# Optimization experiments

Measured on AMD Instinct MI355X. Metric: run time of the kernel, lower is better.

Reference implementation:

```python
import jax, jax.numpy as jnp
import numpy as np

# Module config (from init_kwargs): causal=False, window_size=(256,256), window_type=0,
# softmax_scale=None -> 1/sqrt(D), dropout=0 (eval mode).
WINDOW_LEFT, WINDOW_RIGHT = 256, 256


def _window_mask(Sq, Sk, causal, use_window_mask):
    """Boolean [Sq, Sk] visibility mask, FA2 semantics (right-aligned offset)."""
    qi = jnp.arange(Sq)[:, None]
    kj = jnp.arange(Sk)[None, :]
    offset = Sk - Sq
    if causal:
        return kj <= qi + offset  # window (-1, 0)
    if use_window_mask:
        m = jnp.ones((Sq, Sk), dtype=bool)
        if WINDOW_LEFT >= 0:
            m = m & (kj >= qi + offset - WINDOW_LEFT)
        if WINDOW_RIGHT >= 0:
            m = m & (kj <= qi + offset + WINDOW_RIGHT)
        return m
    return None  # full attention


def setup_inputs() -> dict:
    key = jax.random.key(0)
    kq, kkv = jax.random.split(key)
    B, Sq, Sk, H, D = 2, 2048, 2048, 16, 64
    q = jax.random.normal(kq, (B, Sq, H, D), dtype=jnp.float32)
    kv = jax.random.normal(kkv, (B, Sk, 2, H, D), dtype=jnp.float32)
    return {"q": q, "kv": kv, "causal": 0, "use_window_mask": 1, "return_attn_probs": 0}


def reference(q, kv, causal, use_window_mask, return_attn_probs):
    # q: (B, Sq, H, D); kv: (B, Sk, 2, H, D)
    B, Sq, H, D = q.shape
    Sk = kv.shape[1]
    k = kv[:, :, 0]  # (B, Sk, H, D)
    v = kv[:, :, 1]
    scale = 1.0 / (D ** 0.5)
    scores = jnp.einsum('bqhd,bkhd->bhqk', q, k) * scale  # (B, H, Sq, Sk)
    mask = _window_mask(Sq, Sk, bool(causal), bool(use_window_mask))
    if mask is not None:
        scores = jnp.where(mask[None, None], scores, jnp.finfo(scores.dtype).min)
    probs = jax.nn.softmax(scores, axis=-1)
    out = jnp.einsum('bhqk,bkhd->bqhd', probs, v)  # (B, Sq, H, D)
    return out
```

## Files before the change

### kernel.cpp

```cpp
#include <hip/hip_runtime.h>
#include <hip/hip_bf16.h>

#define B_    2
#define SQ_   2048
#define SK_   2048
#define NH_   16
#define DH_   64
#define WIN_  256
#define NEG_  -30000.0f

typedef __bf16 bf16_t;
typedef bf16_t bf16x8 __attribute__((ext_vector_type(8)));
typedef bf16_t bf16x4 __attribute__((ext_vector_type(4)));
typedef float  f32x4  __attribute__((ext_vector_type(4)));
typedef short  s16x4  __attribute__((ext_vector_type(4)));

#define KSTRIDE 72
#define VSTRIDE 72

__global__ __launch_bounds__(256, 4)
void fa_fwd(const float* __restrict__ qg, const float* __restrict__ kvg,
            float* __restrict__ outg) {
  const int tid  = threadIdx.x;
  const int wid  = tid >> 6;
  const int lane = tid & 63;
  const int quad = lane >> 4;
  const int li   = lane & 15;

  const int bid = blockIdx.x;
  const int qb  = bid >> 5;
  const int bh  = bid & 31;
  const int b   = bh >> 4;
  const int h   = bh & 15;

  const int q0b = qb * 64;
  const int q0  = q0b + wid * 16;

  __shared__ __align__(16) bf16_t sK [2][64 * KSTRIDE];
  __shared__ __align__(16) bf16_t sVT[2][64 * VSTRIDE];

  const float qscale = 0.125f * 1.44269504088896340736f;
  const float* qrow = qg + ((size_t)((b * SQ_ + q0 + li) * NH_ + h)) * DH_;
  bf16x8 qfrag[2];
#pragma unroll
  for (int c = 0; c < 2; ++c) {
    f32x4 a0 = *(const f32x4*)(qrow + c * 32 + quad * 8);
    f32x4 a1 = *(const f32x4*)(qrow + c * 32 + quad * 8 + 4);
#pragma unroll
    for (int i = 0; i < 4; ++i) {
      qfrag[c][i]     = (bf16_t)(a0[i] * qscale);
      qfrag[c][i + 4] = (bf16_t)(a1[i] * qscale);
    }
  }

  f32x4 oacc[4];
#pragma unroll
  for (int t = 0; t < 4; ++t) { f32x4 z = {0.f, 0.f, 0.f, 0.f}; oacc[t] = z; }
  float m = NEG_, l = 0.f;

  int klo = q0b - WIN_; if (klo < 0) klo = 0;
  int khi = q0b + 63 + WIN_ + 1; if (khi > SK_) khi = SK_;
  const int nt = (khi - klo + 63) >> 6;

  const float* kbase = kvg + (size_t)b * SK_ * 2 * NH_ * DH_ + (size_t)h * DH_;
  const float* vbase = kbase + NH_ * DH_;
  const size_t krow_stride = 2 * NH_ * DH_;

  const int skey = tid >> 2;
  const int sd0  = (tid & 3) * 16;

  f32x4 ka[4], va[4];

  auto issue_loads = [&](int kt) {
    const float* kr = kbase + (size_t)(kt + skey) * krow_stride + sd0;
    const float* vr = vbase + (size_t)(kt + skey) * krow_stride + sd0;
#pragma unroll
    for (int i = 0; i < 4; ++i) {
      ka[i] = *(const f32x4*)(kr + 4 * i);
      va[i] = *(const f32x4*)(vr + 4 * i);
    }
  };

  auto stage = [&](int bb) {
#pragma unroll
    for (int hh = 0; hh < 2; ++hh) {
      bf16x8 wk;
#pragma unroll
      for (int i = 0; i < 4; ++i) {
        wk[i] = (bf16_t)ka[2 * hh][i]; wk[i + 4] = (bf16_t)ka[2 * hh + 1][i];
      }
      *(bf16x8*)(&sK[bb][skey * KSTRIDE + sd0 + 8 * hh]) = wk;
      const int dbase = sd0 + 8 * hh;
      const int vcol  = skey ^ (((dbase >> 3) & 7) << 3);
#pragma unroll
      for (int i = 0; i < 4; ++i) {
        sVT[bb][(dbase + i)     * VSTRIDE + vcol] = (bf16_t)va[2 * hh][i];
        sVT[bb][(dbase + 4 + i) * VSTRIDE + vcol] = (bf16_t)va[2 * hh + 1][i];
      }
    }
  };

  issue_loads(klo);
  stage(0);
  if (nt > 1) issue_loads(klo + 64);
  __syncthreads();

  int buf = 0;
  for (int t = 0; t < nt; ++t) {
    const int kk = klo + t * 64;
    if (t + 1 < nt) stage(buf ^ 1);
    if (t + 2 < nt) issue_loads(klo + (t + 2) * 64);

    if (kk + 63 >= q0 - WIN_ && kk <= q0 + 15 + WIN_) {
      f32x4 sc[4];
      __builtin_amdgcn_s_setprio(1);
#pragma unroll
      for (int s = 0; s < 4; ++s) {
        bf16x8 kf0 = *(const bf16x8*)(&sK[buf][(s * 16 + li) * KSTRIDE + quad * 8]);
        bf16x8 kf1 = *(const bf16x8*)(&sK[buf][(s * 16 + li) * KSTRIDE + 32 + quad * 8]);
        f32x4 acc = {0.f, 0.f, 0.f, 0.f};
        acc = __builtin_amdgcn_mfma_f32_16x16x32_bf16(kf0, qfrag[0], acc, 0, 0, 0);
        acc = __builtin_amdgcn_mfma_f32_16x16x32_bf16(kf1, qfrag[1], acc, 0, 0, 0);
        sc[s] = acc;
      }
      __builtin_amdgcn_s_setprio(0);
      if (kk < q0 - 241 || kk > q0 + 193) {
        const int qa = q0 + li;
#pragma unroll
        for (int s = 0; s < 4; ++s)
#pragma unroll
          for (int r = 0; r < 4; ++r) {
            int key = kk + s * 16 + quad * 4 + r;
            unsigned dd = (unsigned)(key - qa + WIN_);
            if (dd > 2u * WIN_) sc[s][r] = NEG_;
          }
      }
      float tl = NEG_;
#pragma unroll
      for (int s = 0; s < 4; ++s)
        tl = fmaxf(tl, fmaxf(fmaxf(sc[s][0], sc[s][1]), fmaxf(sc[s][2], sc[s][3])));

      const bool defer = (__all(tl <= m + 8.0f) != 0);
      float mnew = m;
      if (!defer) {
        float tr = fmaxf(tl, __shfl_xor(tl, 16));
        tr = fmaxf(tr, __shfl_xor(tr, 32));
        mnew = fmaxf(m, tr);
      }

      float psum = 0.f;
      bf16x4 pa[4];
#pragma unroll
      for (int s = 0; s < 4; ++s) {
        float p0 = exp2f(sc[s][0] - mnew);
        float p1 = exp2f(sc[s][1] - mnew);
        float p2 = exp2f(sc[s][2] - mnew);
        float p3 = exp2f(sc[s][3] - mnew);
        psum += (p0 + p1) + (p2 + p3);
        pa[s][0] = (bf16_t)p0; pa[s][1] = (bf16_t)p1;
        pa[s][2] = (bf16_t)p2; pa[s][3] = (bf16_t)p3;
      }

      if (!defer) {
        const float alpha = exp2f(m - mnew);
        float al[4];
#pragma unroll
        for (int r = 0; r < 4; ++r) al[r] = __shfl(alpha, quad * 4 + r);
#pragma unroll
        for (int t2 = 0; t2 < 4; ++t2) {
          oacc[t2][0] *= al[0]; oacc[t2][1] *= al[1];
          oacc[t2][2] *= al[2]; oacc[t2][3] *= al[3];
        }
        l = l * alpha + psum;
        m = mnew;
      } else {
        l += psum;
      }

      __builtin_amdgcn_s_setprio(1);
#pragma unroll
      for (int s = 0; s < 4; ++s) {
        const s16x4 pas = __builtin_bit_cast(s16x4, pa[s]);
#pragma unroll
        for (int t2 = 0; t2 < 4; ++t2) {
          const int d  = 16 * t2 + li;
          const int c8 = ((2 * t2 + (li >> 3)) & 7) << 3;
          s16x4 vb = *(const s16x4*)(&sVT[buf][d * VSTRIDE + ((s * 16 + quad * 4) ^ c8)]);
          oacc[t2] = __builtin_amdgcn_mfma_f32_16x16x16bf16_1k(pas, vb, oacc[t2], 0, 0, 0);
        }
      }
      __builtin_amdgcn_s_setprio(0);
    }

    __syncthreads();
    buf ^= 1;
  }

  l += __shfl_xor(l, 16);
  l += __shfl_xor(l, 32);
  float rl[4];
#pragma unroll
  for (int r = 0; r < 4; ++r) {
    float lv = __shfl(l, quad * 4 + r);
    rl[r] = 1.0f / lv;
  }
  float* orow = outg + ((size_t)((b * SQ_ + q0) * NH_ + h)) * DH_;
#pragma unroll
  for (int t = 0; t < 4; ++t)
#pragma unroll
    for (int r = 0; r < 4; ++r)
      orow[(size_t)(quad * 4 + r) * (NH_ * DH_) + 16 * t + li] = oacc[t][r] * rl[r];
}

extern "C" void kernel_launch(void* const* d_in, const int* in_sizes, int n_in,
                              void* d_out, int out_size, void* d_ws, size_t ws_size,
                              hipStream_t stream) {
  (void)in_sizes; (void)n_in; (void)out_size; (void)d_ws; (void)ws_size;
  const float* q  = (const float*)d_in[0];
  const float* kv = (const float*)d_in[1];
  float* out = (float*)d_out;
  dim3 grid(B_ * NH_ * (SQ_ / 64));
  fa_fwd<<<grid, 256, 0, stream>>>(q, kv, out);
}
```

Baseline: 117.7 us.

## Switch to 32x32x16 MFMA tiles with 128-query blocks and LDS-staged P

Each wave now handles 32 query rows using 32x32x16 bf16 MFMAs for both QK^T and PV, and each block covers 128 queries instead of 64. The P matrix is written to a per-wave LDS buffer and reloaded in operand layout for the PV product. This halves the grid and improves K/V reuse per staged tile while using larger matrix instructions. The cost is extra LDS traffic for P, a lgkmcnt wait, more registers (launch bounds lowered to 2 blocks), and fewer blocks to fill the GPU.

```diff
diff --git a/kernel.cpp b/kernel.cpp
--- a/kernel.cpp
+++ b/kernel.cpp
@@ -13,19 +13,27 @@
 typedef bf16_t bf16x8 __attribute__((ext_vector_type(8)));
 typedef bf16_t bf16x4 __attribute__((ext_vector_type(4)));
 typedef float  f32x4  __attribute__((ext_vector_type(4)));
-typedef short  s16x4  __attribute__((ext_vector_type(4)));
+typedef float  f32x16 __attribute__((ext_vector_type(16)));
 
 #define KSTRIDE 72
 #define VSTRIDE 72
-
-__global__ __launch_bounds__(256, 4)
+#define PSTRIDE 72
+
+static __device__ __forceinline__ f32x16 zero16() {
+  f32x16 z;
+#pragma unroll
+  for (int i = 0; i < 16; ++i) z[i] = 0.f;
+  return z;
+}
+
+__global__ __launch_bounds__(256, 2)
 void fa_fwd(const float* __restrict__ qg, const float* __restrict__ kvg,
             float* __restrict__ outg) {
   const int tid  = threadIdx.x;
   const int wid  = tid >> 6;
   const int lane = tid & 63;
-  const int quad = lane >> 4;
-  const int li   = lane & 15;
+  const int c31  = lane & 31;
+  const int hi   = lane >> 5;
 
   const int bid = blockIdx.x;
   const int qb  = bid >> 5;
@@ -33,33 +41,35 @@
   const int b   = bh >> 4;
   const int h   = bh & 15;
 
-  const int q0b = qb * 64;
-  const int q0  = q0b + wid * 16;
+  const int q0b = qb * 128;
+  const int q0  = q0b + wid * 32;
 
   __shared__ __align__(16) bf16_t sK [2][64 * KSTRIDE];
   __shared__ __align__(16) bf16_t sVT[2][64 * VSTRIDE];
+  __shared__ __align__(16) bf16_t sP [4][32 * PSTRIDE];
+  bf16_t* plw = sP[wid];
 
   const float qscale = 0.125f * 1.44269504088896340736f;
-  const float* qrow = qg + ((size_t)((b * SQ_ + q0 + li) * NH_ + h)) * DH_;
-  bf16x8 qfrag[2];
-#pragma unroll
-  for (int c = 0; c < 2; ++c) {
-    f32x4 a0 = *(const f32x4*)(qrow + c * 32 + quad * 8);
-    f32x4 a1 = *(const f32x4*)(qrow + c * 32 + quad * 8 + 4);
+  const float* qrow = qg + ((size_t)((b * SQ_ + q0 + c31) * NH_ + h)) * DH_;
+  bf16x8 qfrag[4];
+#pragma unroll
+  for (int ds = 0; ds < 4; ++ds) {
+    const int d0 = ds * 16 + hi * 8;
+    f32x4 a0 = *(const f32x4*)(qrow + d0);
+    f32x4 a1 = *(const f32x4*)(qrow + d0 + 4);
 #pragma unroll
     for (int i = 0; i < 4; ++i) {
-      qfrag[c][i]     = (bf16_t)(a0[i] * qscale);
-      qfrag[c][i + 4] = (bf16_t)(a1[i] * qscale);
+      qfrag[ds][i]     = (bf16_t)(a0[i] * qscale);
+      qfrag[ds][i + 4] = (bf16_t)(a1[i] * qscale);
     }
   }
 
-  f32x4 oacc[4];
-#pragma unroll
-  for (int t = 0; t < 4; ++t) { f32x4 z = {0.f, 0.f, 0.f, 0.f}; oacc[t] = z; }
-  float m = NEG_, l = 0.f;
+  f32x16 oacc[2];
+  oacc[0] = zero16(); oacc[1] = zero16();
+  float m = NEG_, el = 0.f;
 
   int klo = q0b - WIN_; if (klo < 0) klo = 0;
-  int khi = q0b + 63 + WIN_ + 1; if (khi > SK_) khi = SK_;
+  int khi = q0b + 127 + WIN_ + 1; if (khi > SK_) khi = SK_;
   const int nt = (khi - klo + 63) >> 6;
 
   const float* kbase = kvg + (size_t)b * SK_ * 2 * NH_ * DH_ + (size_t)h * DH_;
@@ -111,82 +121,96 @@
     if (t + 1 < nt) stage(buf ^ 1);
     if (t + 2 < nt) issue_loads(klo + (t + 2) * 64);
 
-    if (kk + 63 >= q0 - WIN_ && kk <= q0 + 15 + WIN_) {
-      f32x4 sc[4];
+    if (kk + 63 >= q0 - WIN_ && kk <= q0 + 31 + WIN_) {
+      f32x16 sc[2];
       __builtin_amdgcn_s_setprio(1);
 #pragma unroll
-      for (int s = 0; s < 4; ++s) {
-        bf16x8 kf0 = *(const bf16x8*)(&sK[buf][(s * 16 + li) * KSTRIDE + quad * 8]);
-        bf16x8 kf1 = *(const bf16x8*)(&sK[buf][(s * 16 + li) * KSTRIDE + 32 + quad * 8]);
-        f32x4 acc = {0.f, 0.f, 0.f, 0.f};
-        acc = __builtin_amdgcn_mfma_f32_16x16x32_bf16(kf0, qfrag[0], acc, 0, 0, 0);
-        acc = __builtin_amdgcn_mfma_f32_16x16x32_bf16(kf1, qfrag[1], acc, 0, 0, 0);
-        sc[s] = acc;
+      for (int kh = 0; kh < 2; ++kh) {
+        f32x16 acc = zero16();
+#pragma unroll
+        for (int ds = 0; ds < 4; ++ds) {
+          bf16x8 kf = *(const bf16x8*)(
+              &sK[buf][(kh * 32 + c31) * KSTRIDE + ds * 16 + hi * 8]);
+          acc = __builtin_amdgcn_mfma_f32_32x32x16_bf16(kf, qfrag[ds], acc, 0, 0, 0);
+        }
+        sc[kh] = acc;
       }
       __builtin_amdgcn_s_setprio(0);
-      if (kk < q0 - 241 || kk > q0 + 193) {
-        const int qa = q0 + li;
-#pragma unroll
-        for (int s = 0; s < 4; ++s)
-#pragma unroll
-          for (int r = 0; r < 4; ++r) {
-            int key = kk + s * 16 + quad * 4 + r;
+
+      if (kk < q0 - 225 || kk > q0 + 193) {
+        const int qa = q0 + c31;
+#pragma unroll
+        for (int kh = 0; kh < 2; ++kh)
+#pragma unroll
+          for (int r = 0; r < 16; ++r) {
+            int key = kk + kh * 32 + (r & 3) + 8 * (r >> 2) + 4 * hi;
             unsigned dd = (unsigned)(key - qa + WIN_);
-            if (dd > 2u * WIN_) sc[s][r] = NEG_;
+            if (dd > 2u * WIN_) sc[kh][r] = NEG_;
           }
       }
+
       float tl = NEG_;
 #pragma unroll
-      for (int s = 0; s < 4; ++s)
-        tl = fmaxf(tl, fmaxf(fmaxf(sc[s][0], sc[s][1]), fmaxf(sc[s][2], sc[s][3])));
+      for (int kh = 0; kh < 2; ++kh)
+#pragma unroll
+        for (int r = 0; r < 16; r += 4)
+          tl = fmaxf(tl, fmaxf(fmaxf(sc[kh][r], sc[kh][r + 1]),
+                               fmaxf(sc[kh][r + 2], sc[kh][r + 3])));
 
       const bool defer = (__all(tl <= m + 8.0f) != 0);
       float mnew = m;
       if (!defer) {
-        float tr = fmaxf(tl, __shfl_xor(tl, 16));
-        tr = fmaxf(tr, __shfl_xor(tr, 32));
+        float tr = fmaxf(tl, __shfl_xor(tl, 32));
         mnew = fmaxf(m, tr);
       }
 
       float psum = 0.f;
-      bf16x4 pa[4];
-#pragma unroll
-      for (int s = 0; s < 4; ++s) {
-        float p0 = exp2f(sc[s][0] - mnew);
-        float p1 = exp2f(sc[s][1] - mnew);
-        float p2 = exp2f(sc[s][2] - mnew);
-        float p3 = exp2f(sc[s][3] - mnew);
-        psum += (p0 + p1) + (p2 + p3);
-        pa[s][0] = (bf16_t)p0; pa[s][1] = (bf16_t)p1;
-        pa[s][2] = (bf16_t)p2; pa[s][3] = (bf16_t)p3;
-      }
+#pragma unroll
+      for (int kh = 0; kh < 2; ++kh)
+#pragma unroll
+        for (int g = 0; g < 4; ++g) {
+          float p0 = exp2f(sc[kh][4 * g + 0] - mnew);
+          float p1 = exp2f(sc[kh][4 * g + 1] - mnew);
+          float p2 = exp2f(sc[kh][4 * g + 2] - mnew);
+          float p3 = exp2f(sc[kh][4 * g + 3] - mnew);
+          psum += (p0 + p1) + (p2 + p3);
+          bf16x4 pk;
+          pk[0] = (bf16_t)p0; pk[1] = (bf16_t)p1;
+          pk[2] = (bf16_t)p2; pk[3] = (bf16_t)p3;
+          *(bf16x4*)(&plw[c31 * PSTRIDE + kh * 32 + g * 8 + hi * 4]) = pk;
+        }
 
       if (!defer) {
-        const float alpha = exp2f(m - mnew);
-        float al[4];
-#pragma unroll
-        for (int r = 0; r < 4; ++r) al[r] = __shfl(alpha, quad * 4 + r);
-#pragma unroll
-        for (int t2 = 0; t2 < 4; ++t2) {
-          oacc[t2][0] *= al[0]; oacc[t2][1] *= al[1];
-          oacc[t2][2] *= al[2]; oacc[t2][3] *= al[3];
-        }
-        l = l * alpha + psum;
+        const float alq = exp2f(m - mnew);
+#pragma unroll
+        for (int r = 0; r < 16; ++r) {
+          const int row = (r & 3) + 8 * (r >> 2) + 4 * hi;
+          const float al = __shfl(alq, row);
+          oacc[0][r] *= al; oacc[1][r] *= al;
+        }
+        el = el * alq + psum;
         m = mnew;
       } else {
-        l += psum;
-      }
+        el += psum;
+      }
+
+      asm volatile("s_waitcnt lgkmcnt(0)" ::: "memory");
+
+      bf16x8 pf[4];
+#pragma unroll
+      for (int ks = 0; ks < 4; ++ks)
+        pf[ks] = *(const bf16x8*)(&plw[c31 * PSTRIDE + ks * 16 + hi * 8]);
 
       __builtin_amdgcn_s_setprio(1);
 #pragma unroll
-      for (int s = 0; s < 4; ++s) {
-        const s16x4 pas = __builtin_bit_cast(s16x4, pa[s]);
-#pragma unroll
-        for (int t2 = 0; t2 < 4; ++t2) {
-          const int d  = 16 * t2 + li;
-          const int c8 = ((2 * t2 + (li >> 3)) & 7) << 3;
-          s16x4 vb = *(const s16x4*)(&sVT[buf][d * VSTRIDE + ((s * 16 + quad * 4) ^ c8)]);
-          oacc[t2] = __builtin_amdgcn_mfma_f32_16x16x16bf16_1k(pas, vb, oacc[t2], 0, 0, 0);
+      for (int dt = 0; dt < 2; ++dt) {
+        const int d  = dt * 32 + c31;
+        const int c8 = ((d >> 3) & 7) << 3;
+#pragma unroll
+        for (int ks = 0; ks < 4; ++ks) {
+          bf16x8 vf = *(const bf16x8*)(
+              &sVT[buf][d * VSTRIDE + ((ks * 16 + hi * 8) ^ c8)]);
+          oacc[dt] = __builtin_amdgcn_mfma_f32_32x32x16_bf16(pf[ks], vf, oacc[dt], 0, 0, 0);
         }
       }
       __builtin_amdgcn_s_setprio(0);
@@ -196,20 +220,17 @@
     buf ^= 1;
   }
 
-  l += __shfl_xor(l, 16);
-  l += __shfl_xor(l, 32);
-  float rl[4];
-#pragma unroll
-  for (int r = 0; r < 4; ++r) {
-    float lv = __shfl(l, quad * 4 + r);
-    rl[r] = 1.0f / lv;
+  el += __shfl_xor(el, 32);
+  const float rlq = 1.0f / el;
+#pragma unroll
+  for (int r = 0; r < 16; ++r) {
+    const int row = (r & 3) + 8 * (r >> 2) + 4 * hi;
+    const float rl = __shfl(rlq, row);
+    float* orow = outg + ((size_t)((b * SQ_ + q0 + row) * NH_ + h)) * DH_;
+#pragma unroll
+    for (int dt = 0; dt < 2; ++dt)
+      orow[dt * 32 + c31] = oacc[dt][r] * rl;
   }
-  float* orow = outg + ((size_t)((b * SQ_ + q0) * NH_ + h)) * DH_;
-#pragma unroll
-  for (int t = 0; t < 4; ++t)
-#pragma unroll
-    for (int r = 0; r < 4; ++r)
-      orow[(size_t)(quad * 4 + r) * (NH_ * DH_) + 16 * t + li] = oacc[t][r] * rl[r];
 }
 
 extern "C" void kernel_launch(void* const* d_in, const int* in_sizes, int n_in,
@@ -219,6 +240,6 @@
   const float* q  = (const float*)d_in[0];
   const float* kv = (const float*)d_in[1];
   float* out = (float*)d_out;
-  dim3 grid(B_ * NH_ * (SQ_ / 64));
+  dim3 grid(B_ * NH_ * (SQ_ / 128));
   fa_fwd<<<grid, 256, 0, stream>>>(q, kv, out);
 }
```

Result: no change. 116.8 us (-0.8%).

## Pre-convert KV to swizzled bf16 workspace and stream tiles via global_load_lds

Applied to the files above, without the earlier changes.

Adds a prep kernel that converts K and V from fp32 to bf16 once, writing K in an XOR-swizzled row layout and V transposed and swizzled into a workspace buffer. The attention kernel then copies tiles directly into LDS with asynchronous global_load_lds instead of loading fp32 into registers, converting and scattering into LDS on every tile. This removes redundant per-block conversion (each KV tile is read by about nine query blocks) and halves the bytes read in the main kernel. The cost is an extra launch plus a full pass over KV, and the loop now has only one tile of prefetch depth instead of two stages.

```diff
diff --git a/kernel.cpp b/kernel.cpp
--- a/kernel.cpp
+++ b/kernel.cpp
@@ -14,18 +14,56 @@
 typedef bf16_t bf16x4 __attribute__((ext_vector_type(4)));
 typedef float  f32x4  __attribute__((ext_vector_type(4)));
 typedef short  s16x4  __attribute__((ext_vector_type(4)));
-
-#define KSTRIDE 72
-#define VSTRIDE 72
+typedef unsigned int u32;
+
+#define KE_BH 131072
+#define VT_E  4194304
+
+#define GLOAD_LDS16(g, l)                                                      \
+  __builtin_amdgcn_global_load_lds(                                            \
+      (const __attribute__((address_space(1))) u32*)(g),                       \
+      (__attribute__((address_space(3))) u32*)(l), 16, 0, 0)
+
+__global__ __launch_bounds__(256)
+void kv_prep(const float* __restrict__ kvg, bf16_t* __restrict__ wse) {
+  const int t   = blockIdx.x * 256 + threadIdx.x;
+  const int c   = t & 7;
+  const int key = (t >> 3) & (SK_ - 1);
+  const int bh  = t >> 14;
+  const int b   = bh >> 4, h = bh & 15;
+
+  const size_t base =
+      ((((size_t)b * SK_ + key) * 2) * NH_ + h) * (size_t)DH_ + (size_t)(c * 8);
+
+  {
+    f32x4 a0 = *(const f32x4*)(kvg + base);
+    f32x4 a1 = *(const f32x4*)(kvg + base + 4);
+    bf16x8 w;
+#pragma unroll
+    for (int i = 0; i < 4; ++i) { w[i] = (bf16_t)a0[i]; w[i + 4] = (bf16_t)a1[i]; }
+    *(bf16x8*)(wse + (size_t)bh * KE_BH + key * 64 + ((c ^ (key & 7)) << 3)) = w;
+  }
+  {
+    const float* vsrc = kvg + base + NH_ * DH_;
+    const int g = key >> 3, kw = key & 7, gh = g & ~7, gl = g & 7;
+    bf16_t* vdst = wse + VT_E + (size_t)bh * KE_BH + kw;
+#pragma unroll
+    for (int j = 0; j < 8; ++j) {
+      const int d = c * 8 + j;
+      vdst[(size_t)d * 2048 + ((gh | (gl ^ j)) << 3)] = (bf16_t)vsrc[j];
+    }
+  }
+}
 
 __global__ __launch_bounds__(256, 4)
-void fa_fwd(const float* __restrict__ qg, const float* __restrict__ kvg,
+void fa_fwd(const float* __restrict__ qg, const bf16_t* __restrict__ wse,
             float* __restrict__ outg) {
   const int tid  = threadIdx.x;
   const int wid  = tid >> 6;
   const int lane = tid & 63;
   const int quad = lane >> 4;
   const int li   = lane & 15;
+  const int lk   = li & 7;
 
   const int bid = blockIdx.x;
   const int qb  = bid >> 5;
@@ -36,8 +74,11 @@
   const int q0b = qb * 64;
   const int q0  = q0b + wid * 16;
 
-  __shared__ __align__(16) bf16_t sK [2][64 * KSTRIDE];
-  __shared__ __align__(16) bf16_t sVT[2][64 * VSTRIDE];
+  __shared__ __align__(16) bf16_t sK[2][4096];
+  __shared__ __align__(16) bf16_t sV[2][4096];
+
+  const bf16_t* kbh = wse + (size_t)bh * KE_BH;
+  const bf16_t* vbh = wse + VT_E + (size_t)bh * KE_BH;
 
   const float qscale = 0.125f * 1.44269504088896340736f;
   const float* qrow = qg + ((size_t)((b * SQ_ + q0 + li) * NH_ + h)) * DH_;
@@ -62,68 +103,41 @@
   int khi = q0b + 63 + WIN_ + 1; if (khi > SK_) khi = SK_;
   const int nt = (khi - klo + 63) >> 6;
 
-  const float* kbase = kvg + (size_t)b * SK_ * 2 * NH_ * DH_ + (size_t)h * DH_;
-  const float* vbase = kbase + NH_ * DH_;
-  const size_t krow_stride = 2 * NH_ * DH_;
-
-  const int skey = tid >> 2;
-  const int sd0  = (tid & 3) * 16;
-
-  f32x4 ka[4], va[4];
-
-  auto issue_loads = [&](int kt) {
-    const float* kr = kbase + (size_t)(kt + skey) * krow_stride + sd0;
-    const float* vr = vbase + (size_t)(kt + skey) * krow_stride + sd0;
-#pragma unroll
-    for (int i = 0; i < 4; ++i) {
-      ka[i] = *(const f32x4*)(kr + 4 * i);
-      va[i] = *(const f32x4*)(vr + 4 * i);
-    }
-  };
-
-  auto stage = [&](int bb) {
-#pragma unroll
-    for (int hh = 0; hh < 2; ++hh) {
-      bf16x8 wk;
-#pragma unroll
-      for (int i = 0; i < 4; ++i) {
-        wk[i] = (bf16_t)ka[2 * hh][i]; wk[i + 4] = (bf16_t)ka[2 * hh + 1][i];
-      }
-      *(bf16x8*)(&sK[bb][skey * KSTRIDE + sd0 + 8 * hh]) = wk;
-      const int dbase = sd0 + 8 * hh;
-      const int vcol  = skey ^ (((dbase >> 3) & 7) << 3);
-#pragma unroll
-      for (int i = 0; i < 4; ++i) {
-        sVT[bb][(dbase + i)     * VSTRIDE + vcol] = (bf16_t)va[2 * hh][i];
-        sVT[bb][(dbase + 4 + i) * VSTRIDE + vcol] = (bf16_t)va[2 * hh + 1][i];
-      }
-    }
-  };
-
-  issue_loads(klo);
-  stage(0);
-  if (nt > 1) issue_loads(klo + 64);
+  const int tid8 = tid * 8;
+  const int vs0  = (tid >> 3) * 2048 + (tid & 7) * 8;
+
+  GLOAD_LDS16(kbh + klo * 64 + tid8,        &sK[0][tid8]);
+  GLOAD_LDS16(kbh + klo * 64 + 2048 + tid8, &sK[0][2048 + tid8]);
+  GLOAD_LDS16(vbh + klo + vs0,              &sV[0][tid8]);
+  GLOAD_LDS16(vbh + klo + vs0 + 65536,      &sV[0][2048 + tid8]);
   __syncthreads();
 
   int buf = 0;
   for (int t = 0; t < nt; ++t) {
     const int kk = klo + t * 64;
-    if (t + 1 < nt) stage(buf ^ 1);
-    if (t + 2 < nt) issue_loads(klo + (t + 2) * 64);
+    if (t + 1 < nt) {
+      const int kn = kk + 64;
+      GLOAD_LDS16(kbh + kn * 64 + tid8,        &sK[buf ^ 1][tid8]);
+      GLOAD_LDS16(kbh + kn * 64 + 2048 + tid8, &sK[buf ^ 1][2048 + tid8]);
+      GLOAD_LDS16(vbh + kn + vs0,              &sV[buf ^ 1][tid8]);
+      GLOAD_LDS16(vbh + kn + vs0 + 65536,      &sV[buf ^ 1][2048 + tid8]);
+    }
 
     if (kk + 63 >= q0 - WIN_ && kk <= q0 + 15 + WIN_) {
       f32x4 sc[4];
       __builtin_amdgcn_s_setprio(1);
 #pragma unroll
       for (int s = 0; s < 4; ++s) {
-        bf16x8 kf0 = *(const bf16x8*)(&sK[buf][(s * 16 + li) * KSTRIDE + quad * 8]);
-        bf16x8 kf1 = *(const bf16x8*)(&sK[buf][(s * 16 + li) * KSTRIDE + 32 + quad * 8]);
+        const int row = (s * 16 + li) * 64;
+        bf16x8 kf0 = *(const bf16x8*)(&sK[buf][row + ((quad ^ lk) << 3)]);
+        bf16x8 kf1 = *(const bf16x8*)(&sK[buf][row + (((quad + 4) ^ lk) << 3)]);
         f32x4 acc = {0.f, 0.f, 0.f, 0.f};
         acc = __builtin_amdgcn_mfma_f32_16x16x32_bf16(kf0, qfrag[0], acc, 0, 0, 0);
         acc = __builtin_amdgcn_mfma_f32_16x16x32_bf16(kf1, qfrag[1], acc, 0, 0, 0);
         sc[s] = acc;
       }
       __builtin_amdgcn_s_setprio(0);
+
       if (kk < q0 - 241 || kk > q0 + 193) {
         const int qa = q0 + li;
 #pragma unroll
@@ -181,11 +195,12 @@
 #pragma unroll
       for (int s = 0; s < 4; ++s) {
         const s16x4 pas = __builtin_bit_cast(s16x4, pa[s]);
+        const int cA = 2 * s + (quad >> 1);
 #pragma unroll
         for (int t2 = 0; t2 < 4; ++t2) {
-          const int d  = 16 * t2 + li;
-          const int c8 = ((2 * t2 + (li >> 3)) & 7) << 3;
-          s16x4 vb = *(const s16x4*)(&sVT[buf][d * VSTRIDE + ((s * 16 + quad * 4) ^ c8)]);
+          const int d = 16 * t2 + li;
+          s16x4 vb = *(const s16x4*)(
+              &sV[buf][d * 64 + ((cA ^ lk) << 3) + (quad & 1) * 4]);
           oacc[t2] = __builtin_amdgcn_mfma_f32_16x16x16bf16_1k(pas, vb, oacc[t2], 0, 0, 0);
         }
       }
@@ -215,10 +230,12 @@
 extern "C" void kernel_launch(void* const* d_in, const int* in_sizes, int n_in,
                               void* d_out, int out_size, void* d_ws, size_t ws_size,
                               hipStream_t stream) {
-  (void)in_sizes; (void)n_in; (void)out_size; (void)d_ws; (void)ws_size;
+  (void)in_sizes; (void)n_in; (void)out_size; (void)ws_size;
   const float* q  = (const float*)d_in[0];
   const float* kv = (const float*)d_in[1];
   float* out = (float*)d_out;
-  dim3 grid(B_ * NH_ * (SQ_ / 64));
-  fa_fwd<<<grid, 256, 0, stream>>>(q, kv, out);
+  bf16_t* wse = (bf16_t*)d_ws;
+
+  kv_prep<<<dim3(2048), 256, 0, stream>>>(kv, wse);
+  fa_fwd<<<dim3(B_ * NH_ * (SQ_ / 64)), 256, 0, stream>>>(q, wse, out);
 }
```

Result: slower. 125.8 us (+6.9%).
